# Kernel tuning notes

Hardware: AMD Instinct MI355X
Metric: run time of the kernel (lower is better)

## Reference

```python
import jax, jax.numpy as jnp
import numpy as np

N_NODES = 50000
N_EDGES = 800000
IN_DIM = 128
HID = 128
N_POS = 100000


def setup_inputs() -> dict:
    key = jax.random.key(0)
    ks = jax.random.split(key, 16)
    inp = {
        "adj_indices": jax.random.randint(ks[0], (N_EDGES, 2), 0, N_NODES, dtype=jnp.int64)
        if jax.config.jax_enable_x64 else jax.random.randint(ks[0], (N_EDGES, 2), 0, N_NODES, dtype=jnp.int32),
        "adj_values": jax.random.uniform(ks[1], (N_EDGES,), dtype=jnp.float32),
        "num_nodes": N_NODES,
        "h": jax.random.normal(ks[2], (N_NODES, IN_DIM), dtype=jnp.float32),
        "pos_u": jax.random.randint(ks[3], (N_POS,), 0, N_NODES),
        "pos_v": jax.random.randint(ks[4], (N_POS,), 0, N_NODES),
        "neg_u": jax.random.randint(ks[5], (N_POS,), 0, N_NODES),
        "neg_v": jax.random.randint(ks[6], (N_POS,), 0, N_NODES),
    }
    # learned parameters (torch Linear: y = x @ W + b with W stored as [in, out] here)
    s1 = 1.0 / np.sqrt(IN_DIM)
    s2 = 1.0 / np.sqrt(HID)
    sd = 1.0 / np.sqrt(2 * HID)
    inp["W1"] = jax.random.uniform(ks[7], (IN_DIM, HID), minval=-s1, maxval=s1, dtype=jnp.float32)
    inp["b1"] = jax.random.uniform(ks[8], (HID,), minval=-s1, maxval=s1, dtype=jnp.float32)
    inp["W2"] = jax.random.uniform(ks[9], (HID, HID), minval=-s2, maxval=s2, dtype=jnp.float32)
    inp["b2"] = jax.random.uniform(ks[10], (HID,), minval=-s2, maxval=s2, dtype=jnp.float32)
    inp["Wd1"] = jax.random.uniform(ks[11], (2 * HID, HID), minval=-sd, maxval=sd, dtype=jnp.float32)
    inp["bd1"] = jax.random.uniform(ks[12], (HID,), minval=-sd, maxval=sd, dtype=jnp.float32)
    inp["Wd2"] = jax.random.uniform(ks[13], (HID, 1), minval=-s2, maxval=s2, dtype=jnp.float32)
    inp["bd2"] = jax.random.uniform(ks[14], (1,), minval=-s2, maxval=s2, dtype=jnp.float32)
    return inp


def reference(adj_indices, adj_values, num_nodes, h, pos_u, pos_v, neg_u, neg_v,
              W1, b1, W2, b2, Wd1, bd1, Wd2, bd2):
    row = adj_indices[:, 0]
    col = adj_indices[:, 1]
    # degree = rowwise sum of sparse values, clamped at 1
    deg = jnp.clip(jax.ops.segment_sum(adj_values, row, num_segments=num_nodes), 1.0, None)
    deg_inv = (1.0 / deg)[:, None]  # [N, 1]

    def spmm(x):  # A @ x via gather-scale-scatter over edge list
        return jax.ops.segment_sum(adj_values[:, None] * x[col], row, num_segments=num_nodes)

    h1 = jax.nn.relu((spmm(h) * deg_inv) @ W1 + b1)        # [N, HID]
    h2 = (spmm(h1) * deg_inv) @ W2 + b2                    # [N, HID]

    def decode(u, v):
        z = jnp.concatenate([h2[u], h2[v]], axis=1)        # [P, 2*HID]
        return (jax.nn.relu(z @ Wd1 + bd1) @ Wd2 + bd2)[:, 0]

    pos_scores = decode(pos_u, pos_v)
    neg_scores = decode(neg_u, neg_v)
    return pos_scores, neg_scores, h2
```

## Files before the change

kernel.cpp:

```cpp
#include <hip/hip_runtime.h>


typedef float  f32x4 __attribute__((ext_vector_type(4)));
typedef short  s16x8 __attribute__((ext_vector_type(8)));
typedef short  s16x4 __attribute__((ext_vector_type(4)));

__device__ inline short f2bf(float f){
  union { float f; unsigned u; } x; x.f = f;
  unsigned u = x.u;
  return (short)((u + 0x7FFFu + ((u >> 16) & 1u)) >> 16);
}
__device__ inline float bf2f(short h){
  union { unsigned u; float f; } c; c.u = ((unsigned)(unsigned short)h) << 16;
  return c.f;
}

__global__ void k_count(const int* __restrict__ idx, int* __restrict__ cnt, int E){
  int e = blockIdx.x*blockDim.x + threadIdx.x;
  if (e >= E) return;
  int2 rc = ((const int2*)idx)[e];
  atomicAdd(&cnt[rc.x], 1);
}

__global__ void k_blocksum(const int* __restrict__ rp, int* __restrict__ bsum, int N){
  int i = blockIdx.x*256 + threadIdx.x;
  int c = (i < N) ? rp[i] : 0;
  #pragma unroll
  for (int off = 1; off < 64; off <<= 1) c += __shfl_xor(c, off);
  __shared__ int s[4];
  if ((threadIdx.x & 63) == 0) s[threadIdx.x >> 6] = c;
  __syncthreads();
  if (threadIdx.x == 0) bsum[blockIdx.x] = s[0] + s[1] + s[2] + s[3];
}

__global__ void k_scanb(const int* __restrict__ bsum, int* __restrict__ boff,
                        int* __restrict__ rpN, int B){
  __shared__ int s[256];
  int t = threadIdx.x;
  int run = 0;
  for (int base = 0; base < B; base += 256){
    int c = (base + t < B) ? bsum[base + t] : 0;
    s[t] = c;
    __syncthreads();
    #pragma unroll
    for (int off = 1; off < 256; off <<= 1){
      int v = s[t];
      int u = (t >= off) ? s[t-off] : 0;
      __syncthreads();
      s[t] = v + u;
      __syncthreads();
    }
    if (base + t < B) boff[base + t] = run + s[t] - c;
    run += s[255];
    __syncthreads();
  }
  if (t == 0) rpN[0] = run;
}

__global__ void k_addoff(int* __restrict__ rp, int* __restrict__ cursor,
                         const int* __restrict__ boff, int N){
  __shared__ int s[256];
  int t = threadIdx.x;
  int i = blockIdx.x*256 + t;
  int c = (i < N) ? rp[i] : 0;
  s[t] = c;
  __syncthreads();
  #pragma unroll
  for (int off = 1; off < 256; off <<= 1){
    int v = s[t];
    int u = (t >= off) ? s[t-off] : 0;
    __syncthreads();
    s[t] = v + u;
    __syncthreads();
  }
  int excl = s[t] - c + boff[blockIdx.x];
  if (i < N){ rp[i] = excl; cursor[i] = excl; }
}

__global__ void k_scatter(const int* __restrict__ idx, const float* __restrict__ vals,
                          int* __restrict__ cursor, int2* __restrict__ ce, int E){
  int e = blockIdx.x*blockDim.x + threadIdx.x;
  if (e >= E) return;
  int2 rc = ((const int2*)idx)[e];
  int p = atomicAdd(&cursor[rc.x], 1);
  ce[p] = make_int2(rc.y, __float_as_int(vals[e]));
}

__global__ void k_prep(const float* __restrict__ h, const float* __restrict__ W1,
                       const float* __restrict__ W2, const float* __restrict__ Wd1,
                       short* __restrict__ hb, short* __restrict__ Wh,
                       short* __restrict__ Wl, short* __restrict__ WdP, int n4){
  int gid = blockIdx.x*256 + threadIdx.x;
  if (gid < n4){
    float4 v = ((const float4*)h)[gid];
    s16x4 o; o[0]=f2bf(v.x); o[1]=f2bf(v.y); o[2]=f2bf(v.z); o[3]=f2bf(v.w);
    *(s16x4*)&hb[(size_t)gid*4] = o;
  } else if (gid < n4 + 32768){
    int idx = gid - n4;
    int b = idx & 7, lane = (idx >> 3) & 63, kk = (idx >> 9) & 3, j = (idx >> 11) & 7;
    int m = idx >> 14;
    const float* W = m ? W2 : W1;
    int row = kk*32 + 8*(lane >> 4) + b;
    int col = j*16 + (lane & 15);
    float x = W[row*128 + col];
    short hbit = f2bf(x);
    Wh[idx] = hbit;
    Wl[idx] = f2bf(x - bf2f(hbit));
  } else if (gid < n4 + 65536){
    int idx = gid - n4 - 32768;
    int b = idx & 7, lane = (idx >> 3) & 63, kk = (idx >> 9) & 7, j = (idx >> 12) & 7;
    int row = kk*32 + 8*(lane >> 4) + b;
    int col = j*16 + (lane & 15);
    WdP[idx] = f2bf(Wd1[row*128 + col]);
  }
}

__global__ void k_spmm(const int* __restrict__ rp, const int2* __restrict__ ce,
                       const short* __restrict__ Xb, float* __restrict__ out, int N){
  int r = blockIdx.x*16 + (threadIdx.x >> 4);
  int t = threadIdx.x & 15;
  if (r >= N) return;
  f32x4 a0 = {0.f,0.f,0.f,0.f}, a1 = {0.f,0.f,0.f,0.f};
  float vs0 = 0.f, vs1 = 0.f;
  int e0 = rp[r], e1 = rp[r+1];
  int e = e0;
  for (; e + 3 < e1; e += 4){
    int2 p0 = ce[e], p1 = ce[e+1], p2 = ce[e+2], p3 = ce[e+3];
    s16x8 x0 = *(const s16x8*)&Xb[(size_t)p0.x*128 + t*8];
    s16x8 x1 = *(const s16x8*)&Xb[(size_t)p1.x*128 + t*8];
    s16x8 x2 = *(const s16x8*)&Xb[(size_t)p2.x*128 + t*8];
    s16x8 x3 = *(const s16x8*)&Xb[(size_t)p3.x*128 + t*8];
    float v0 = __int_as_float(p0.y), v1 = __int_as_float(p1.y);
    float v2 = __int_as_float(p2.y), v3 = __int_as_float(p3.y);
    #pragma unroll
    for (int b = 0; b < 4; ++b){
      a0[b] = fmaf(v0, bf2f(x0[b]), a0[b]);   a1[b] = fmaf(v0, bf2f(x0[b+4]), a1[b]);
      a0[b] = fmaf(v1, bf2f(x1[b]), a0[b]);   a1[b] = fmaf(v1, bf2f(x1[b+4]), a1[b]);
      a0[b] = fmaf(v2, bf2f(x2[b]), a0[b]);   a1[b] = fmaf(v2, bf2f(x2[b+4]), a1[b]);
      a0[b] = fmaf(v3, bf2f(x3[b]), a0[b]);   a1[b] = fmaf(v3, bf2f(x3[b+4]), a1[b]);
    }
    vs0 += v0 + v2; vs1 += v1 + v3;
  }
  for (; e < e1; ++e){
    int2 p0 = ce[e];
    s16x8 x0 = *(const s16x8*)&Xb[(size_t)p0.x*128 + t*8];
    float v0 = __int_as_float(p0.y);
    #pragma unroll
    for (int b = 0; b < 4; ++b){
      a0[b] = fmaf(v0, bf2f(x0[b]), a0[b]);
      a1[b] = fmaf(v0, bf2f(x0[b+4]), a1[b]);
    }
    vs0 += v0;
  }
  float di = 1.0f / fmaxf(vs0 + vs1, 1.0f);
  a0 *= di; a1 *= di;
  *(f32x4*)&out[(size_t)r*128 + t*8]     = a0;
  *(f32x4*)&out[(size_t)r*128 + t*8 + 4] = a1;
}

template<bool RELU, bool EMIT_F32, bool EMIT_BF16>
__global__ __launch_bounds__(256)
void k_mgemm(const float* __restrict__ A, const short* __restrict__ Wh,
             const short* __restrict__ Wl, const float* __restrict__ bias,
             float* __restrict__ out, short* __restrict__ out_bf, int M)
{
  const int wave = threadIdx.x >> 6;
  const int lane = threadIdx.x & 63;
  const int l15 = lane & 15, lg = lane >> 4;
  const int wrow = blockIdx.x*64 + wave*16;
  int arow = wrow + l15; if (arow >= M) arow = M - 1;

  s16x8 ah[4], al[4];
  #pragma unroll
  for (int kk = 0; kk < 4; ++kk){
    const float* src = &A[(size_t)arow*128 + kk*32 + 8*lg];
    float4 x0 = *(const float4*)src;
    float4 x1 = *(const float4*)(src + 4);
    float xs[8] = {x0.x,x0.y,x0.z,x0.w,x1.x,x1.y,x1.z,x1.w};
    #pragma unroll
    for (int b = 0; b < 8; ++b){
      short hb = f2bf(xs[b]);
      ah[kk][b] = hb;
      al[kk][b] = f2bf(xs[b] - bf2f(hb));
    }
  }

  const s16x8* WH = (const s16x8*)Wh;
  const s16x8* WL = (const s16x8*)Wl;
  f32x4 acc[8];
  #pragma unroll
  for (int j = 0; j < 8; ++j) acc[j] = (f32x4){0.f,0.f,0.f,0.f};

  #pragma unroll
  for (int j = 0; j < 8; ++j){
    #pragma unroll
    for (int kk = 0; kk < 4; ++kk){
      s16x8 bh = WH[(j*4 + kk)*64 + lane];
      s16x8 bl = WL[(j*4 + kk)*64 + lane];
      acc[j] = __builtin_amdgcn_mfma_f32_16x16x32_bf16(ah[kk], bh, acc[j], 0, 0, 0);
      acc[j] = __builtin_amdgcn_mfma_f32_16x16x32_bf16(al[kk], bh, acc[j], 0, 0, 0);
      acc[j] = __builtin_amdgcn_mfma_f32_16x16x32_bf16(ah[kk], bl, acc[j], 0, 0, 0);
    }
  }

  #pragma unroll
  for (int j = 0; j < 8; ++j){
    int col = j*16 + l15;
    float bb = bias[col];
    #pragma unroll
    for (int r = 0; r < 4; ++r){
      int row = wrow + 4*lg + r;
      if (row < M){
        float v = acc[j][r] + bb;
        if (RELU) v = fmaxf(v, 0.f);
        if (EMIT_F32)  out[(size_t)row*128 + col] = v;
        if (EMIT_BF16) out_bf[(size_t)row*128 + col] = f2bf(v);
      }
    }
  }
}

__global__ __launch_bounds__(256)
void k_decode(const short* __restrict__ h2b, const short* __restrict__ WdP,
              const float* __restrict__ bd1, const float* __restrict__ wd2,
              const float* __restrict__ bd2,
              const int* __restrict__ pos_u, const int* __restrict__ pos_v,
              const int* __restrict__ neg_u, const int* __restrict__ neg_v,
              float* __restrict__ out_pos, float* __restrict__ out_neg, int P)
{
  __shared__ short Bs[32768];

  const int which = blockIdx.y;
  const int* iu = which ? neg_u : pos_u;
  const int* iv = which ? neg_v : pos_v;
  float* out = which ? out_neg : out_pos;

  const int wave = threadIdx.x >> 6;
  const int lane = threadIdx.x & 63;
  const int l15 = lane & 15, lg = lane >> 4;
  const int wbase = blockIdx.x*128 + wave*32;

  int ra0 = wbase + l15;      if (ra0 >= P) ra0 = P - 1;
  int ra1 = wbase + 16 + l15; if (ra1 >= P) ra1 = P - 1;
  int u0 = iu[ra0], v0 = iv[ra0];
  int u1 = iu[ra1], v1 = iv[ra1];

  s16x8 a0[8], a1[8];
  #pragma unroll
  for (int kk = 0; kk < 8; ++kk){
    int kg = kk*32 + 8*lg;
    const short* s0 = (kg < 128) ? h2b + (size_t)u0*128 + kg
                                 : h2b + (size_t)v0*128 + (kg - 128);
    const short* s1 = (kg < 128) ? h2b + (size_t)u1*128 + kg
                                 : h2b + (size_t)v1*128 + (kg - 128);
    a0[kk] = *(const s16x8*)s0;
    a1[kk] = *(const s16x8*)s1;
  }

  {
    const int4* src = (const int4*)WdP;
    int4* dst = (int4*)Bs;
    #pragma unroll
    for (int i = 0; i < 16; ++i)
      dst[threadIdx.x + i*256] = src[threadIdx.x + i*256];
  }
  __syncthreads();

  const s16x8* Wp = (const s16x8*)Bs;
  f32x4 acc0[8], acc1[8];
  #pragma unroll
  for (int j = 0; j < 8; ++j){
    acc0[j] = (f32x4){0.f,0.f,0.f,0.f};
    acc1[j] = (f32x4){0.f,0.f,0.f,0.f};
  }

  #pragma unroll
  for (int j = 0; j < 8; ++j){
    #pragma unroll
    for (int kk = 0; kk < 8; ++kk){
      s16x8 b = Wp[(j*8 + kk)*64 + lane];
      acc0[j] = __builtin_amdgcn_mfma_f32_16x16x32_bf16(a0[kk], b, acc0[j], 0, 0, 0);
      acc1[j] = __builtin_amdgcn_mfma_f32_16x16x32_bf16(a1[kk], b, acc1[j], 0, 0, 0);
    }
  }

  float part0[4] = {0,0,0,0}, part1[4] = {0,0,0,0};
  #pragma unroll
  for (int j = 0; j < 8; ++j){
    int col = j*16 + l15;
    float bb = bd1[col], ww = wd2[col];
    #pragma unroll
    for (int r = 0; r < 4; ++r){
      part0[r] = fmaf(fmaxf(acc0[j][r] + bb, 0.f), ww, part0[r]);
      part1[r] = fmaf(fmaxf(acc1[j][r] + bb, 0.f), ww, part1[r]);
    }
  }
  #pragma unroll
  for (int off = 1; off < 16; off <<= 1){
    #pragma unroll
    for (int r = 0; r < 4; ++r){
      part0[r] += __shfl_xor(part0[r], off);
      part1[r] += __shfl_xor(part1[r], off);
    }
  }
  if (l15 == 0){
    float b2v = bd2[0];
    int m0 = wbase + 4*lg, m1 = wbase + 16 + 4*lg;
    #pragma unroll
    for (int r = 0; r < 4; ++r){
      if (m0 + r < P) out[m0 + r] = part0[r] + b2v;
      if (m1 + r < P) out[m1 + r] = part1[r] + b2v;
    }
  }
}

extern "C" void kernel_launch(void* const* d_in, const int* in_sizes, int n_in,
                              void* d_out, int out_size, void* d_ws, size_t ws_size,
                              hipStream_t stream){
  const int*   adj   = (const int*)  d_in[0];
  const float* av    = (const float*)d_in[1];
  const float* h     = (const float*)d_in[3];
  const int*   pos_u = (const int*)  d_in[4];
  const int*   pos_v = (const int*)  d_in[5];
  const int*   neg_u = (const int*)  d_in[6];
  const int*   neg_v = (const int*)  d_in[7];
  const float* W1    = (const float*)d_in[8];
  const float* b1    = (const float*)d_in[9];
  const float* W2    = (const float*)d_in[10];
  const float* b2    = (const float*)d_in[11];
  const float* Wd1   = (const float*)d_in[12];
  const float* bd1   = (const float*)d_in[13];
  const float* Wd2   = (const float*)d_in[14];
  const float* bd2   = (const float*)d_in[15];

  const int E = in_sizes[0] / 2;
  const int N = in_sizes[3] / 128;
  const int P = in_sizes[4];
  const int NB = (N + 255) / 256;
  const int n4 = N * 128 / 4;

  auto al = [](size_t x){ return (x + 255) & ~(size_t)255; };
  char* base = (char*)d_ws;
  size_t off = 0;
  int*   rp     = (int*)(base + off);   off = al(off + (size_t)(N+1)*4);
  int*   cursor = (int*)(base + off);   off = al(off + (size_t)N*4);
  int*   bsum   = (int*)(base + off);   off = al(off + (size_t)NB*4);
  int*   boff   = (int*)(base + off);   off = al(off + (size_t)NB*4);
  int2*  ce     = (int2*)(base + off);  off = al(off + (size_t)E*8);
  short* W12h   = (short*)(base + off); off = al(off + (size_t)32768*2);
  short* W12l   = (short*)(base + off); off = al(off + (size_t)32768*2);
  short* WdP    = (short*)(base + off); off = al(off + (size_t)32768*2);
  short* hb     = (short*)(base + off); off = al(off + (size_t)N*128*2);
  short* h1b    = (short*)(base + off); off = al(off + (size_t)N*128*2);
  short* h2b    = (short*)(base + off); off = al(off + (size_t)N*128*2);

  float* scores_pos = (float*)d_out;
  float* scores_neg = scores_pos + P;
  float* h2         = scores_neg + P;

  hipMemsetAsync(rp, 0, (size_t)(N+1)*4, stream);

  k_count   <<<(E+255)/256, 256, 0, stream>>>(adj, rp, E);
  k_blocksum<<<NB, 256, 0, stream>>>(rp, bsum, N);
  k_scanb   <<<1, 256, 0, stream>>>(bsum, boff, rp + N, NB);
  k_addoff  <<<NB, 256, 0, stream>>>(rp, cursor, boff, N);
  k_scatter <<<(E+255)/256, 256, 0, stream>>>(adj, av, cursor, ce, E);
  k_prep    <<<(n4 + 65536 + 255)/256, 256, 0, stream>>>(h, W1, W2, Wd1, hb, W12h, W12l, WdP, n4);

  k_spmm<<<(N+15)/16, 256, 0, stream>>>(rp, ce, hb, h2, N);
  k_mgemm<true , false, true ><<<(N+63)/64, 256, 0, stream>>>(h2, W12h, W12l, b1, nullptr, h1b, N);

  k_spmm<<<(N+15)/16, 256, 0, stream>>>(rp, ce, h1b, h2, N);
  k_mgemm<false, true , true ><<<(N+63)/64, 256, 0, stream>>>(h2, W12h + 16384, W12l + 16384, b2, h2, h2b, N);

  dim3 dgrid((P+127)/128, 2);
  k_decode<<<dgrid, 256, 0, stream>>>(h2b, WdP, bd1, Wd2, bd2,
                                      pos_u, pos_v, neg_u, neg_v,
                                      scores_pos, scores_neg, P);
}
```

Before: 333.2 us.

## Record per-edge rank during counting to drop second atomic pass in CSR build

The count kernel now keeps the value returned by its atomicAdd as a per-edge rank. The scatter kernel then places each edge at rp[row] + rank with no atomics, and the separate cursor array goes away. Both kernels also process four edges per thread with the loads batched, to raise memory-level parallelism. The cost is an extra E-sized rank array that is written once and read once.

```diff
diff --git a/kernel.cpp b/kernel.cpp
--- a/kernel.cpp
+++ b/kernel.cpp
@@ -15,11 +15,24 @@
   return c.f;
 }
 
-__global__ void k_count(const int* __restrict__ idx, int* __restrict__ cnt, int E){
-  int e = blockIdx.x*blockDim.x + threadIdx.x;
-  if (e >= E) return;
-  int2 rc = ((const int2*)idx)[e];
-  atomicAdd(&cnt[rc.x], 1);
+__global__ void k_count(const int* __restrict__ idx, int* __restrict__ cnt,
+                        int* __restrict__ rank, int E, int S){
+  int i = blockIdx.x*256 + threadIdx.x;
+  int e0 = i, e1 = i + S, e2 = i + 2*S, e3 = i + 3*S;
+  int2 rc0, rc1, rc2, rc3;
+  if (e0 < E) rc0 = ((const int2*)idx)[e0];
+  if (e1 < E) rc1 = ((const int2*)idx)[e1];
+  if (e2 < E) rc2 = ((const int2*)idx)[e2];
+  if (e3 < E) rc3 = ((const int2*)idx)[e3];
+  int r0 = 0, r1 = 0, r2 = 0, r3 = 0;
+  if (e0 < E) r0 = atomicAdd(&cnt[rc0.x], 1);
+  if (e1 < E) r1 = atomicAdd(&cnt[rc1.x], 1);
+  if (e2 < E) r2 = atomicAdd(&cnt[rc2.x], 1);
+  if (e3 < E) r3 = atomicAdd(&cnt[rc3.x], 1);
+  if (e0 < E) rank[e0] = r0;
+  if (e1 < E) rank[e1] = r1;
+  if (e2 < E) rank[e2] = r2;
+  if (e3 < E) rank[e3] = r3;
 }
 
 __global__ void k_blocksum(const int* __restrict__ rp, int* __restrict__ bsum, int N){
@@ -57,8 +70,7 @@
   if (t == 0) rpN[0] = run;
 }
 
-__global__ void k_addoff(int* __restrict__ rp, int* __restrict__ cursor,
-                         const int* __restrict__ boff, int N){
+__global__ void k_addoff(int* __restrict__ rp, const int* __restrict__ boff, int N){
   __shared__ int s[256];
   int t = threadIdx.x;
   int i = blockIdx.x*256 + t;
@@ -73,17 +85,22 @@
     s[t] = v + u;
     __syncthreads();
   }
-  int excl = s[t] - c + boff[blockIdx.x];
-  if (i < N){ rp[i] = excl; cursor[i] = excl; }
+  if (i < N) rp[i] = s[t] - c + boff[blockIdx.x];
 }
 
 __global__ void k_scatter(const int* __restrict__ idx, const float* __restrict__ vals,
-                          int* __restrict__ cursor, int2* __restrict__ ce, int E){
-  int e = blockIdx.x*blockDim.x + threadIdx.x;
-  if (e >= E) return;
-  int2 rc = ((const int2*)idx)[e];
-  int p = atomicAdd(&cursor[rc.x], 1);
-  ce[p] = make_int2(rc.y, __float_as_int(vals[e]));
+                          const int* __restrict__ rp, const int* __restrict__ rank,
+                          int2* __restrict__ ce, int E, int S){
+  int i = blockIdx.x*256 + threadIdx.x;
+  #pragma unroll
+  for (int q = 0; q < 4; ++q){
+    int e = i + q*S;
+    if (e < E){
+      int2 rc = ((const int2*)idx)[e];
+      int p = rp[rc.x] + rank[e];
+      ce[p] = make_int2(rc.y, __float_as_int(vals[e]));
+    }
+  }
 }
 
 __global__ void k_prep(const float* __restrict__ h, const float* __restrict__ W1,
@@ -343,7 +360,7 @@
   char* base = (char*)d_ws;
   size_t off = 0;
   int*   rp     = (int*)(base + off);   off = al(off + (size_t)(N+1)*4);
-  int*   cursor = (int*)(base + off);   off = al(off + (size_t)N*4);
+  int*   rank   = (int*)(base + off);   off = al(off + (size_t)E*4);
   int*   bsum   = (int*)(base + off);   off = al(off + (size_t)NB*4);
   int*   boff   = (int*)(base + off);   off = al(off + (size_t)NB*4);
   int2*  ce     = (int2*)(base + off);  off = al(off + (size_t)E*8);
@@ -360,11 +377,13 @@
 
   hipMemsetAsync(rp, 0, (size_t)(N+1)*4, stream);
 
-  k_count   <<<(E+255)/256, 256, 0, stream>>>(adj, rp, E);
+  const int EG = ((E + 3) / 4 + 255) / 256;
+  const int S  = EG * 256;
+  k_count   <<<EG, 256, 0, stream>>>(adj, rp, rank, E, S);
   k_blocksum<<<NB, 256, 0, stream>>>(rp, bsum, N);
   k_scanb   <<<1, 256, 0, stream>>>(bsum, boff, rp + N, NB);
-  k_addoff  <<<NB, 256, 0, stream>>>(rp, cursor, boff, N);
-  k_scatter <<<(E+255)/256, 256, 0, stream>>>(adj, av, cursor, ce, E);
+  k_addoff  <<<NB, 256, 0, stream>>>(rp, boff, N);
+  k_scatter <<<EG, 256, 0, stream>>>(adj, av, rp, rank, ce, E, S);
   k_prep    <<<(n4 + 65536 + 255)/256, 256, 0, stream>>>(h, W1, W2, Wd1, hb, W12h, W12l, WdP, n4);
 
   k_spmm<<<(N+15)/16, 256, 0, stream>>>(rp, ce, hb, h2, N);
```

Result: faster. 308.6 us (-7.4%).
